# Kernel optimization log

Measured on AMD Instinct MI355X. Metric: run time of the kernel, lower is better.

## Reference

```python
import jax, jax.numpy as jnp
import numpy as np


def setup_inputs() -> dict:
    key = jax.random.key(0)
    k1, k2 = jax.random.split(key)
    B, C, H, W = 16, 8, 512, 512
    pred_logits = jax.random.normal(k1, (B, C, H, W), dtype=jnp.float32)
    target_mask = (jax.random.uniform(k2, (B, C, H, W)) < 0.1).astype(jnp.float32)
    return {"pred_logits": pred_logits, "target_mask": target_mask}


def _induction_map(target_mask):
    # Vectorized replacement of the per-slice nonzero().mean() loop:
    # for each (b,c) slice, put a 1 at the (floor) centroid of nonzero pixels.
    B, C, H, W = target_mask.shape
    w = (target_mask != 0).astype(jnp.float32)          # [B,C,H,W]
    cnt = w.sum(axis=(-2, -1))                           # [B,C]
    rows = jnp.arange(H, dtype=jnp.float32)
    cols = jnp.arange(W, dtype=jnp.float32)
    rsum = (w.sum(axis=-1) * rows).sum(axis=-1)          # [B,C] sum of row idx over nonzeros
    csum = (w.sum(axis=-2) * cols).sum(axis=-1)          # [B,C] sum of col idx over nonzeros
    safe = jnp.maximum(cnt, 1.0)
    mid_r = (rsum / safe).astype(jnp.int32)              # torch .int() truncation (coords >= 0)
    mid_c = (csum / safe).astype(jnp.int32)
    has = cnt > 0                                        # [B,C]
    oh_r = jnp.arange(H)[None, None, :] == mid_r[..., None]   # [B,C,H]
    oh_c = jnp.arange(W)[None, None, :] == mid_c[..., None]   # [B,C,W]
    ind = oh_r[..., :, None] & oh_c[..., None, :] & has[..., None, None]
    return ind.astype(target_mask.dtype)                 # [B,C,H,W]


def reference(pred_logits, target_mask):
    z = _induction_map(jax.lax.stop_gradient(target_mask))
    x = pred_logits
    # BCEWithLogits (stable form), mean reduction
    loss = jnp.maximum(x, 0.0) - x * z + jnp.log1p(jnp.exp(-jnp.abs(x)))
    return loss.mean()
```

## Files before the change

kernel.cpp:

```cpp
#include <hip/hip_runtime.h>
#include <math.h>

#define BB 16
#define CC 8
#define HH 512
#define WW 512
#define SLICES (BB*CC)
#define SLICE_ELEMS (HH*WW)
#define BLOCKS_PER_SLICE 16
#define CHUNK (SLICE_ELEMS/BLOCKS_PER_SLICE)
#define NBLOCKS (SLICES*BLOCKS_PER_SLICE)
#define NTHREADS 256
#define TOTAL_N ((long long)SLICES*SLICE_ELEMS)

#define WS_CNT_OFF   0
#define WS_RSUM_OFF  (SLICES)
#define WS_CSUM_OFF  (2*SLICES)
#define WS_INT_BYTES (3*SLICES*sizeof(int))
#define WS_PARTIAL_BYTE_OFF WS_INT_BYTES

#define LOG2E 1.44269504088896340736f
#define LN2   0.69314718055994530942f

__device__ __forceinline__ float softplus_term(float x) {
    float a = fabsf(x);
    float t = __builtin_amdgcn_exp2f(-a * LOG2E);
    float l = __builtin_amdgcn_logf(1.0f + t);
    return fmaxf(x, 0.0f) + LN2 * l;
}

__global__ __launch_bounds__(NTHREADS) void pil_main(
    const float* __restrict__ logits,
    const float* __restrict__ mask,
    int* __restrict__ cnt, int* __restrict__ rsum, int* __restrict__ csum,
    double* __restrict__ partial)
{
    const int blk      = blockIdx.x;
    const int slice    = blk / BLOCKS_PER_SLICE;
    const int subchunk = blk % BLOCKS_PER_SLICE;
    const int chunkStartInSlice = subchunk * CHUNK;
    const long long base = (long long)slice * SLICE_ELEMS + chunkStartInSlice;
    const int tid = threadIdx.x;

    const float4* m4 = reinterpret_cast<const float4*>(mask + base);
    const float4* x4 = reinterpret_cast<const float4*>(logits + base);

    int    c_loc = 0, r_loc = 0, col_loc = 0;
    double s_loc = 0.0;

    for (int i = tid; i < CHUNK / 4; i += NTHREADS) {
        float4 m = m4[i];
        float4 x = x4[i];
        int eInSlice = chunkStartInSlice + i * 4;
        int row = eInSlice >> 9;
        int col = eInSlice & 511;

        int m0 = (m.x != 0.0f);
        int m1 = (m.y != 0.0f);
        int m2 = (m.z != 0.0f);
        int m3 = (m.w != 0.0f);
        int msum = m0 + m1 + m2 + m3;
        c_loc   += msum;
        r_loc   += row * msum;
        col_loc += col * msum + m1 + 2 * m2 + 3 * m3;

        float f = softplus_term(x.x) + softplus_term(x.y)
                + softplus_term(x.z) + softplus_term(x.w);
        s_loc += (double)f;
    }

    for (int off = 32; off > 0; off >>= 1) {
        c_loc   += __shfl_down(c_loc,   off);
        r_loc   += __shfl_down(r_loc,   off);
        col_loc += __shfl_down(col_loc, off);
        s_loc   += __shfl_down(s_loc,   off);
    }

    __shared__ int    sc[NTHREADS / 64], sr[NTHREADS / 64], scol[NTHREADS / 64];
    __shared__ double sd[NTHREADS / 64];
    const int wave = tid >> 6;
    const int lane = tid & 63;
    if (lane == 0) { sc[wave] = c_loc; sr[wave] = r_loc; scol[wave] = col_loc; sd[wave] = s_loc; }
    __syncthreads();

    if (tid == 0) {
        int    bc = 0, br = 0, bcol = 0;
        double bs = 0.0;
        #pragma unroll
        for (int w = 0; w < NTHREADS / 64; ++w) { bc += sc[w]; br += sr[w]; bcol += scol[w]; bs += sd[w]; }
        atomicAdd(&cnt[slice],  bc);
        atomicAdd(&rsum[slice], br);
        atomicAdd(&csum[slice], bcol);
        partial[blk] = bs;
    }
}

__global__ __launch_bounds__(NTHREADS) void pil_final(
    const float* __restrict__ logits,
    const int* __restrict__ cnt, const int* __restrict__ rsum, const int* __restrict__ csum,
    const double* __restrict__ partial,
    float* __restrict__ out)
{
    __shared__ double sdata[NTHREADS];
    const int tid = threadIdx.x;

    double s = 0.0;
    for (int i = tid; i < NBLOCKS; i += NTHREADS) s += partial[i];

    if (tid < SLICES) {
        int c = cnt[tid];
        if (c > 0) {
            int mr = (int)((float)rsum[tid] / (float)c);
            int mc = (int)((float)csum[tid] / (float)c);
            s -= (double)logits[(long long)tid * SLICE_ELEMS + (long long)mr * WW + mc];
        }
    }

    sdata[tid] = s;
    __syncthreads();
    for (int stride = NTHREADS / 2; stride > 0; stride >>= 1) {
        if (tid < stride) sdata[tid] += sdata[tid + stride];
        __syncthreads();
    }
    if (tid == 0) out[0] = (float)(sdata[0] / (double)TOTAL_N);
}

extern "C" void kernel_launch(void* const* d_in, const int* in_sizes, int n_in,
                              void* d_out, int out_size, void* d_ws, size_t ws_size,
                              hipStream_t stream)
{
    const float* logits = (const float*)d_in[0];
    const float* mask   = (const float*)d_in[1];
    float* out = (float*)d_out;

    int*    ws_int     = (int*)d_ws;
    int*    cnt        = ws_int + WS_CNT_OFF;
    int*    rsum       = ws_int + WS_RSUM_OFF;
    int*    csum       = ws_int + WS_CSUM_OFF;
    double* partial    = (double*)((char*)d_ws + WS_PARTIAL_BYTE_OFF);

    hipMemsetAsync(d_ws, 0, WS_INT_BYTES, stream);

    pil_main<<<NBLOCKS, NTHREADS, 0, stream>>>(logits, mask, cnt, rsum, csum, partial);
    pil_final<<<1, NTHREADS, 0, stream>>>(logits, cnt, rsum, csum, partial, out);
}
```

Baseline: 54.98 us.

## Replace per-slice atomics and memset with per-block partials; unroll loads by four

Each block now writes its count, row-sum and column-sum to per-block workspace slots instead of using atomicAdd into per-slice counters. The final kernel sums the 16 partials per slice, so the hipMemsetAsync launch before the main kernel is no longer needed. The main loop is also unrolled four ways with all loads issued up front to raise memory-level parallelism. This costs more registers per thread and slightly more work in the single-block final kernel.

```diff
diff --git a/kernel.cpp b/kernel.cpp
--- a/kernel.cpp
+++ b/kernel.cpp
@@ -13,11 +13,10 @@
 #define NTHREADS 256
 #define TOTAL_N ((long long)SLICES*SLICE_ELEMS)
 
-#define WS_CNT_OFF   0
-#define WS_RSUM_OFF  (SLICES)
-#define WS_CSUM_OFF  (2*SLICES)
-#define WS_INT_BYTES (3*SLICES*sizeof(int))
-#define WS_PARTIAL_BYTE_OFF WS_INT_BYTES
+#define WS_PARTIAL_OFF 0
+#define WS_PC_BYTE_OFF   (NBLOCKS * sizeof(double))
+#define WS_PR_BYTE_OFF   (WS_PC_BYTE_OFF + NBLOCKS * sizeof(int))
+#define WS_PCOL_BYTE_OFF (WS_PR_BYTE_OFF + NBLOCKS * sizeof(int))
 
 #define LOG2E 1.44269504088896340736f
 #define LN2   0.69314718055994530942f
@@ -32,8 +31,8 @@
 __global__ __launch_bounds__(NTHREADS) void pil_main(
     const float* __restrict__ logits,
     const float* __restrict__ mask,
-    int* __restrict__ cnt, int* __restrict__ rsum, int* __restrict__ csum,
-    double* __restrict__ partial)
+    double* __restrict__ partial,
+    int* __restrict__ pc, int* __restrict__ pr, int* __restrict__ pcol)
 {
     const int blk      = blockIdx.x;
     const int slice    = blk / BLOCKS_PER_SLICE;
@@ -48,25 +47,38 @@
     int    c_loc = 0, r_loc = 0, col_loc = 0;
     double s_loc = 0.0;
 
-    for (int i = tid; i < CHUNK / 4; i += NTHREADS) {
-        float4 m = m4[i];
-        float4 x = x4[i];
-        int eInSlice = chunkStartInSlice + i * 4;
-        int row = eInSlice >> 9;
-        int col = eInSlice & 511;
+    for (int i0 = tid; i0 < CHUNK / 4; i0 += 4 * NTHREADS) {
+        float4 ma = m4[i0];
+        float4 mb = m4[i0 + NTHREADS];
+        float4 mc = m4[i0 + 2 * NTHREADS];
+        float4 md = m4[i0 + 3 * NTHREADS];
+        float4 xa = x4[i0];
+        float4 xb = x4[i0 + NTHREADS];
+        float4 xc = x4[i0 + 2 * NTHREADS];
+        float4 xd = x4[i0 + 3 * NTHREADS];
 
-        int m0 = (m.x != 0.0f);
-        int m1 = (m.y != 0.0f);
-        int m2 = (m.z != 0.0f);
-        int m3 = (m.w != 0.0f);
-        int msum = m0 + m1 + m2 + m3;
-        c_loc   += msum;
-        r_loc   += row * msum;
-        col_loc += col * msum + m1 + 2 * m2 + 3 * m3;
+        #pragma unroll
+        for (int u = 0; u < 4; ++u) {
+            float4 m = (u == 0) ? ma : (u == 1) ? mb : (u == 2) ? mc : md;
+            float4 x = (u == 0) ? xa : (u == 1) ? xb : (u == 2) ? xc : xd;
+            int i = i0 + u * NTHREADS;
+            int eInSlice = chunkStartInSlice + i * 4;
+            int row = eInSlice >> 9;
+            int col = eInSlice & 511;
 
-        float f = softplus_term(x.x) + softplus_term(x.y)
-                + softplus_term(x.z) + softplus_term(x.w);
-        s_loc += (double)f;
+            int m0 = (m.x != 0.0f);
+            int m1 = (m.y != 0.0f);
+            int m2 = (m.z != 0.0f);
+            int m3 = (m.w != 0.0f);
+            int msum = m0 + m1 + m2 + m3;
+            c_loc   += msum;
+            r_loc   += row * msum;
+            col_loc += col * msum + m1 + 2 * m2 + 3 * m3;
+
+            float f = softplus_term(x.x) + softplus_term(x.y)
+                    + softplus_term(x.z) + softplus_term(x.w);
+            s_loc += (double)f;
+        }
     }
 
     for (int off = 32; off > 0; off >>= 1) {
@@ -88,17 +100,17 @@
         double bs = 0.0;
         #pragma unroll
         for (int w = 0; w < NTHREADS / 64; ++w) { bc += sc[w]; br += sr[w]; bcol += scol[w]; bs += sd[w]; }
-        atomicAdd(&cnt[slice],  bc);
-        atomicAdd(&rsum[slice], br);
-        atomicAdd(&csum[slice], bcol);
+        pc[blk]      = bc;
+        pr[blk]      = br;
+        pcol[blk]    = bcol;
         partial[blk] = bs;
     }
 }
 
 __global__ __launch_bounds__(NTHREADS) void pil_final(
     const float* __restrict__ logits,
-    const int* __restrict__ cnt, const int* __restrict__ rsum, const int* __restrict__ csum,
     const double* __restrict__ partial,
+    const int* __restrict__ pc, const int* __restrict__ pr, const int* __restrict__ pcol,
     float* __restrict__ out)
 {
     __shared__ double sdata[NTHREADS];
@@ -108,10 +120,17 @@
     for (int i = tid; i < NBLOCKS; i += NTHREADS) s += partial[i];
 
     if (tid < SLICES) {
-        int c = cnt[tid];
+        int c = 0, r = 0, cl = 0;
+        #pragma unroll
+        for (int k = 0; k < BLOCKS_PER_SLICE; ++k) {
+            int idx = tid * BLOCKS_PER_SLICE + k;
+            c  += pc[idx];
+            r  += pr[idx];
+            cl += pcol[idx];
+        }
         if (c > 0) {
-            int mr = (int)((float)rsum[tid] / (float)c);
-            int mc = (int)((float)csum[tid] / (float)c);
+            int mr = (int)((float)r  / (float)c);
+            int mc = (int)((float)cl / (float)c);
             s -= (double)logits[(long long)tid * SLICE_ELEMS + (long long)mr * WW + mc];
         }
     }
@@ -133,14 +152,11 @@
     const float* mask   = (const float*)d_in[1];
     float* out = (float*)d_out;
 
-    int*    ws_int     = (int*)d_ws;
-    int*    cnt        = ws_int + WS_CNT_OFF;
-    int*    rsum       = ws_int + WS_RSUM_OFF;
-    int*    csum       = ws_int + WS_CSUM_OFF;
-    double* partial    = (double*)((char*)d_ws + WS_PARTIAL_BYTE_OFF);
+    double* partial = (double*)((char*)d_ws + WS_PARTIAL_OFF);
+    int*    pc      = (int*)((char*)d_ws + WS_PC_BYTE_OFF);
+    int*    pr      = (int*)((char*)d_ws + WS_PR_BYTE_OFF);
+    int*    pcol    = (int*)((char*)d_ws + WS_PCOL_BYTE_OFF);
 
-    hipMemsetAsync(d_ws, 0, WS_INT_BYTES, stream);
-
-    pil_main<<<NBLOCKS, NTHREADS, 0, stream>>>(logits, mask, cnt, rsum, csum, partial);
-    pil_final<<<1, NTHREADS, 0, stream>>>(logits, cnt, rsum, csum, partial, out);
+    pil_main<<<NBLOCKS, NTHREADS, 0, stream>>>(logits, mask, partial, pc, pr, pcol);
+    pil_final<<<1, NTHREADS, 0, stream>>>(logits, partial, pc, pr, pcol, out);
 }
```

New measurement: 49.98 us. -9.1%, faster.
